# Kernel tuning notes

Measured on AMD Instinct MI355X. Metric: run time of the kernel, lower is better.

## Reference

```python
import jax, jax.numpy as jnp
import numpy as np

N, T, E, E2 = 10000, 32, 320000, 160000
D, H = 128, 128
SLOPE = 0.01  # LeakyReLU negative slope (args.relu)


def _lstm_dir(x, mask, Wih, Whh, b, reverse):
    # x: [N,T,D], mask: [N,T] int; returns final hidden [N,H] honoring per-seq lengths
    xs = jnp.swapaxes(x, 0, 1)                                 # [T,N,D]
    ms = jnp.swapaxes(mask, 0, 1)[..., None].astype(x.dtype)   # [T,N,1]
    Hh = Whh.shape[1]
    h0 = jnp.zeros((x.shape[0], Hh), x.dtype)

    def step(carry, tm):
        h, c = carry
        xt, mt = tm
        g = xt @ Wih.T + h @ Whh.T + b                         # [N,4H], torch gate order i,f,g,o
        i, f, gg, o = jnp.split(g, 4, axis=-1)
        i, f, o = jax.nn.sigmoid(i), jax.nn.sigmoid(f), jax.nn.sigmoid(o)
        c_new = f * c + i * jnp.tanh(gg)
        h_new = o * jnp.tanh(c_new)
        h = mt * h_new + (1.0 - mt) * h
        c = mt * c_new + (1.0 - mt) * c
        return (h, c), None

    (h, _), _ = jax.lax.scan(step, (h0, h0), (xs, ms), reverse=reverse)
    return h


def _sage(h, src, dst, Wself, Wneigh, b):
    # DGL SAGEConv, mean aggregator: h@W_self + mean_neigh(h)@W_neigh + b
    n = h.shape[0]
    msum = jax.ops.segment_sum(h[src], dst, num_segments=n)
    deg = jax.ops.segment_sum(jnp.ones((src.shape[0],), h.dtype), dst, num_segments=n)
    neigh = msum / jnp.maximum(deg, 1.0)[:, None]
    return h @ Wself + neigh @ Wneigh + b


def setup_inputs():
    key = jax.random.key(0)
    ks = jax.random.split(key, 40)
    f = lambda i, shape: jax.random.normal(ks[i], shape, jnp.float32) * 0.05
    return dict(
        inputs_s=jax.random.randint(ks[0], (N, T), 0, 128, jnp.int32),
        inputs_sm=jnp.ones((N, T), jnp.int32),
        inputs_c=jax.random.randint(ks[1], (N,), 0, 101, jnp.int32),
        inputs_co=jax.random.randint(ks[2], (N,), 0, 92, jnp.int32),
        inputs_sl=jax.random.randint(ks[3], (N,), 0, 6, jnp.int32),
        inputs_ip=jax.random.normal(ks[4], (N, 32), jnp.float32),
        blk_src=jax.random.randint(ks[5], (E,), 0, N, jnp.int32),
        blk_dst=jax.random.randint(ks[6], (E,), 0, N, jnp.int32),
        e_src=jax.random.randint(ks[7], (E2,), 0, N, jnp.int32),
        e_dst=jax.random.randint(ks[8], (E2,), 0, N, jnp.int32),
        emb_url=f(9, (128, D)), emb_cat=f(10, (101, D)), emb_cou=f(11, (92, D)), emb_sl_t=f(12, (6, D)),
        Wih_f=f(13, (4 * D, D)), Whh_f=f(14, (4 * D, D)), b_f=f(15, (4 * D,)),
        Wih_b=f(16, (4 * D, D)), Whh_b=f(17, (4 * D, D)), b_b=f(18, (4 * D,)),
        fc_lstm_W=f(19, (2 * D, D)), fc_lstm_b=f(20, (D,)),
        attnlin_W=f(21, (H, H)), attn_W=f(22, (H, 1)), attn_b=f(23, (1,)),
        W0_self=f(24, (4, D, H)), W0_neigh=f(25, (4, D, H)), b0=f(26, (4, H)),
        Wip_self=f(27, (32, H)), Wip_neigh=f(28, (32, H)), bip=f(29, (H,)),
        W1_self=f(30, (5, H, H)), W1_neigh=f(31, (5, H, H)), b1=f(32, (5, H)),
        fc_W=f(33, (2 * H, H)), fc_b=f(34, (H,)),
        fco_W=f(35, (H, 2)), fco_b=f(36, (2,)),
    )


def reference(inputs_s, inputs_sm, inputs_c, inputs_co, inputs_sl, inputs_ip,
              blk_src, blk_dst, e_src, e_dst,
              emb_url, emb_cat, emb_cou, emb_sl_t,
              Wih_f, Whh_f, b_f, Wih_b, Whh_b, b_b,
              fc_lstm_W, fc_lstm_b, attnlin_W, attn_W, attn_b,
              W0_self, W0_neigh, b0, Wip_self, Wip_neigh, bip,
              W1_self, W1_neigh, b1, fc_W, fc_b, fco_W, fco_b):
    lrelu = lambda x: jax.nn.leaky_relu(x, SLOPE)
    # --- URL encoder: embed -> bi-LSTM -> fc (dropout is identity in eval) ---
    xu = emb_url[inputs_s]                                      # [N,T,D]
    hf = _lstm_dir(xu, inputs_sm, Wih_f, Whh_f, b_f, False)     # fwd final hidden
    hb = _lstm_dir(xu, inputs_sm, Wih_b, Whh_b, b_b, True)      # bwd final hidden
    vec_url = lrelu(jnp.concatenate([hf, hb], 1) @ fc_lstm_W + fc_lstm_b)
    # --- six-stream (here five: no rules) SAGE stacks over shared blocks ---
    h4 = jnp.stack([vec_url, emb_cat[inputs_c], emb_cou[inputs_co], emb_sl_t[inputs_sl]])  # [4,N,D]
    sage_v = jax.vmap(_sage, in_axes=(0, None, None, 0, 0, 0))
    h4 = lrelu(sage_v(h4, blk_src, blk_dst, W0_self, W0_neigh, b0))
    hip = lrelu(_sage(inputs_ip, blk_src, blk_dst, Wip_self, Wip_neigh, bip))
    hs = jnp.concatenate([h4, hip[None]], 0)                    # [5,N,H]
    hs = lrelu(sage_v(hs, blk_src, blk_dst, W1_self, W1_neigh, b1))
    hs = jnp.transpose(hs, (1, 0, 2))                           # [N,5,H]
    # --- attention fusion across streams ---
    z = jnp.einsum('nsh,ho->nso', hs, attnlin_W)                # attn_linear(h_stack)
    a = jax.nn.softmax(jnp.einsum('nso,om->nsm', z, attn_W) + attn_b, axis=1)  # [N,5,1]
    h = jnp.sum(z * a, axis=1)                                  # [N,H]
    # --- per-edge gather-concat-MLP scoring (apply_edges) ---
    cat = jnp.concatenate([h[e_src], h[e_dst]], 1)              # [E2,2H]
    score = lrelu(cat @ fc_W + fc_b) @ fco_W + fco_b            # [E2,2]
    a_src = a[e_src][..., 0]                                    # [E2,5]
    attn_e = jnp.stack([a_src, a_src], axis=1)                  # [E2,2,5]
    return score, attn_e
```

## Files before the change

### kernel.cpp

```cpp
#include <hip/hip_runtime.h>
#include <hip/hip_bf16.h>
#include <stdint.h>

typedef unsigned short u16;
typedef unsigned int   u32;
typedef __attribute__((ext_vector_type(8))) short short8;
typedef __attribute__((ext_vector_type(4))) float f32x4;
typedef __attribute__((ext_vector_type(2))) u32   u32x2;
typedef __attribute__((ext_vector_type(4))) u32   u32x4;

#define DEV static __device__ __forceinline__

constexpr int N_  = 10000;
constexpr int T_  = 32;
constexpr int E_  = 320000;
constexpr int E2_ = 160000;

DEV u16 f2bf(float f) {
    union { float f; u32 u; } v; v.f = f;
    u32 u = v.u;
    return (u16)((u + 0x7fffu + ((u >> 16) & 1u)) >> 16);
}
DEV float bf2f(u16 h) {
    union { u32 u; float f; } v; v.u = ((u32)h) << 16; return v.f;
}
DEV float asf(u32 u) {
    union { u32 u; float f; } v; v.u = u; return v.f;
}
DEV u32 cvt_pk_bf16(float lo, float hi) {
    u32 r;
    asm("v_cvt_pk_bf16_f32 %0, %1, %2" : "=v"(r) : "v"(lo), "v"(hi));
    return r;
}
DEV float lrelu(float x) { return x > 0.f ? x : 0.01f * x; }

DEV float fexp2(float x) {
#if __has_builtin(__builtin_amdgcn_exp2f)
    return __builtin_amdgcn_exp2f(x);
#else
    return exp2f(x);
#endif
}
DEV float frcp(float x) {
#if __has_builtin(__builtin_amdgcn_rcpf)
    return __builtin_amdgcn_rcpf(x);
#else
    return 1.0f / x;
#endif
}
DEV float fsig(float x)  { return frcp(1.f + fexp2(-1.4426950408889634f * x)); }
DEV float ftanh_(float x){ return 1.f - 2.f * frcp(1.f + fexp2(2.8853900817779268f * x)); }

__global__ void k_xtab(const float* __restrict__ emb,
                       const float* __restrict__ WihF, const float* __restrict__ bF,
                       const float* __restrict__ WihB, const float* __restrict__ bB,
                       u16* __restrict__ xtab) {
    int sym = blockIdx.x, dir = blockIdx.y, o = threadIdx.x;
    const float* W = dir ? WihB : WihF;
    const float* b = dir ? bB : bF;
    __shared__ float er[128];
    if (o < 128) er[o] = emb[sym * 128 + o];
    __syncthreads();
    float s = b[o];
    const float4* Wr = (const float4*)(W + (size_t)o * 128);
    for (int k4 = 0; k4 < 32; k4++) {
        float4 wv = Wr[k4];
        s += er[4*k4]   * wv.x + er[4*k4+1] * wv.y
           + er[4*k4+2] * wv.z + er[4*k4+3] * wv.w;
    }
    xtab[((size_t)(dir * 128 + sym)) * 512 + o] = f2bf(s);
}

struct WtSeg { const float* W; u16* out; int Kd, Ks, Nw, tot; };
struct WtArgs {
    WtSeg seg[9];
    int* deg; float* bias5; const float* b0; const float* bip;
};
__global__ void k_wt_all(WtArgs a) {
    if (blockIdx.y == 9) {
        int gid = blockIdx.x * 256 + threadIdx.x;
        if (gid < N_) a.deg[gid] = 0;
        int b = gid - 10240;
        if (b >= 0 && b < 640) a.bias5[b] = (b < 512) ? a.b0[b] : a.bip[b - 512];
        return;
    }
    WtSeg sg = a.seg[blockIdx.y];
    int i = blockIdx.x * 256 + threadIdx.x;
    if (i >= sg.tot) return;
    int k = i % sg.Kd, n = (i / sg.Kd) % sg.Nw, s = i / (sg.Kd * sg.Nw);
    float v = (k < sg.Ks) ? sg.W[((size_t)s * sg.Ks + k) * sg.Nw + n] : 0.f;
    sg.out[i] = f2bf(v);
}

__global__ __launch_bounds__(512, 2) void k_lstm(
    const u16* __restrict__ xtab,
    const int* __restrict__ syms,
    const int* __restrict__ smask,
    const float* __restrict__ WhhF,
    const float* __restrict__ WhhB,
    u16* __restrict__ hcat)
{
    __shared__ u16 h_buf0[2048];
    __shared__ u16 h_buf1[2048];
    __shared__ int sym_l[512];
    __shared__ int msk_l[512];

    int tid = threadIdx.x;
    int w = tid >> 6, l = tid & 63, l15 = l & 15, lg = l >> 4;
    int dir = blockIdx.y;
    int n0 = blockIdx.x * 16;
    const float* Whh = dir ? WhhB : WhhF;

    for (int i = tid; i < 512; i += 512) {
        int seq = i >> 5, t = i & 31;
        sym_l[t * 16 + seq] = syms[(size_t)n0 * 32 + i];
        msk_l[t * 16 + seq] = smask[(size_t)n0 * 32 + i];
    }
    for (int i = tid; i < 2048; i += 512) h_buf0[i] = 0;

    short8 aw[4][4];
#pragma unroll
    for (int gg = 0; gg < 4; gg++)
#pragma unroll
    for (int kk = 0; kk < 4; kk++) {
        const float* p = Whh + (size_t)(128 * gg + 16 * w + l15) * 128 + 32 * kk + 8 * lg;
        const float4* pp = (const float4*)p;
        float4 x0 = pp[0], x1 = pp[1];
        short8 v;
        v[0] = (short)f2bf(x0.x); v[1] = (short)f2bf(x0.y);
        v[2] = (short)f2bf(x0.z); v[3] = (short)f2bf(x0.w);
        v[4] = (short)f2bf(x1.x); v[5] = (short)f2bf(x1.y);
        v[6] = (short)f2bf(x1.z); v[7] = (short)f2bf(x1.w);
        aw[gg][kk] = v;
    }

    float hreg[4] = {0, 0, 0, 0};
    float creg[4] = {0, 0, 0, 0};
    int jb = 16 * w + 4 * lg;
    int wsk = 2 * w + (lg >> 1);
    int wof = (wsk * 16 + l15) * 8 + 4 * (lg & 1);
    const u16* xbase = xtab + (size_t)dir * 128 * 512 + jb;
    __syncthreads();

    u32x2 xt[4];
    {
        int t0 = dir ? 31 : 0;
        int sym0 = sym_l[t0 * 16 + l15];
        const u16* xr = xbase + (size_t)sym0 * 512;
#pragma unroll
        for (int gg = 0; gg < 4; gg++) xt[gg] = *(const u32x2*)(xr + gg * 128);
    }

    auto step = [&](int st, const u16* rb, u16* wb, bool wr) {
        int t = dir ? (31 - st) : st;

        short8 bh[4];
#pragma unroll
        for (int kk = 0; kk < 4; kk++)
            bh[kk] = *(const short8*)&rb[((kk * 4 + lg) * 16 + l15) * 8];

        f32x4 acc[4];
#pragma unroll
        for (int gg = 0; gg < 4; gg++) {
            f32x4 a = { asf(xt[gg][0] << 16), asf(xt[gg][0] & 0xffff0000u),
                        asf(xt[gg][1] << 16), asf(xt[gg][1] & 0xffff0000u) };
#pragma unroll
            for (int kk = 0; kk < 4; kk++)
                a = __builtin_amdgcn_mfma_f32_16x16x32_bf16(aw[gg][kk], bh[kk], a, 0, 0, 0);
            acc[gg] = a;
        }

        if (wr) {
            int stn = st + 1;
            int tn = dir ? (31 - stn) : stn;
            int symn = sym_l[tn * 16 + l15];
            const u16* xr = xbase + (size_t)symn * 512;
#pragma unroll
            for (int gg = 0; gg < 4; gg++) xt[gg] = *(const u32x2*)(xr + gg * 128);
        }

        int mt_i = msk_l[t * 16 + l15];
        bool mb = mt_i != 0;
#pragma unroll
        for (int r = 0; r < 4; r++) {
            float i_ = fsig(acc[0][r]), f_ = fsig(acc[1][r]);
            float g_ = ftanh_(acc[2][r]), o_ = fsig(acc[3][r]);
            float cn = f_ * creg[r] + i_ * g_;
            float hn = o_ * ftanh_(cn);
            hreg[r] = mb ? hn : hreg[r];
            creg[r] = mb ? cn : creg[r];
        }
        if (wr) {
            u32x2 pk;
            pk[0] = cvt_pk_bf16(hreg[0], hreg[1]);
            pk[1] = cvt_pk_bf16(hreg[2], hreg[3]);
            *(u32x2*)&wb[wof] = pk;
            asm volatile("s_waitcnt lgkmcnt(0)" ::: "memory");
            __builtin_amdgcn_s_barrier();
        }
    };

    for (int st2 = 0; st2 < 15; st2++) {
        step(2 * st2,     h_buf0, h_buf1, true);
        step(2 * st2 + 1, h_buf1, h_buf0, true);
    }
    step(30, h_buf0, h_buf1, true);
    step(31, h_buf1, h_buf0, false);

    {
        u32x2 pk;
        pk[0] = cvt_pk_bf16(hreg[0], hreg[1]);
        pk[1] = cvt_pk_bf16(hreg[2], hreg[3]);
        *(u32x2*)&hcat[(size_t)(n0 + l15) * 256 + dir * 128 + jb] = pk;
    }
}

template<int ACT, int DUAL>
__global__ __launch_bounds__(256) void k_gemm(
    const u16* __restrict__ A1, int lda1, int soA1,
    const u16* __restrict__ A2, int lda2, int soA2,
    const u16* __restrict__ B1, int soB1,
    const u16* __restrict__ B2, int soB2,
    const float* __restrict__ bias, int soBias,
    u16* __restrict__ C, int ldc, int soC, int M, int K)
{
    int s = blockIdx.y;
    A1 += (size_t)s * soA1;
    if (DUAL) A2 += (size_t)s * soA2;
    B1 += (size_t)s * soB1;
    if (DUAL) B2 += (size_t)s * soB2;
    if (bias) bias += (size_t)s * soBias;
    C += (size_t)s * soC;

    int tid = threadIdx.x;
    int w = tid >> 6, l = tid & 63, l15 = l & 15, lg = l >> 4;
    int mbase = blockIdx.x * 64 + w * 16;
    int arow = mbase + l15; if (arow >= M) arow = M - 1;

    f32x4 acc[8];
#pragma unroll
    for (int nt = 0; nt < 8; nt++) {
        float bv = bias ? bias[16 * nt + l15] : 0.f;
        acc[nt] = (f32x4){bv, bv, bv, bv};
    }
    for (int k0 = 0; k0 < K; k0 += 32) {
        int k = k0 + 8 * lg;
        short8 a1 = *(const short8*)&A1[(size_t)arow * lda1 + k];
        short8 a2;
        if (DUAL) a2 = *(const short8*)&A2[(size_t)arow * lda2 + k];
#pragma unroll
        for (int nt = 0; nt < 8; nt++) {
            short8 b1 = *(const short8*)&B1[(size_t)(16 * nt + l15) * K + k];
            acc[nt] = __builtin_amdgcn_mfma_f32_16x16x32_bf16(a1, b1, acc[nt], 0, 0, 0);
            if (DUAL) {
                short8 b2 = *(const short8*)&B2[(size_t)(16 * nt + l15) * K + k];
                acc[nt] = __builtin_amdgcn_mfma_f32_16x16x32_bf16(a2, b2, acc[nt], 0, 0, 0);
            }
        }
    }
#pragma unroll
    for (int nt = 0; nt < 8; nt++)
#pragma unroll
    for (int r = 0; r < 4; r++) {
        int m = mbase + 4 * lg + r;
        if (m < M) {
            float v = acc[nt][r];
            if (ACT == 1) v = lrelu(v);
            C[(size_t)m * ldc + 16 * nt + l15] = f2bf(v);
        }
    }
}

__global__ __launch_bounds__(256) void k_fcpack(
    const u16* __restrict__ hcat, const u16* __restrict__ Bt,
    const float* __restrict__ bias, u16* __restrict__ F0,
    const int* __restrict__ ic, const int* __restrict__ ico,
    const int* __restrict__ isl, const float* __restrict__ ip,
    const float* __restrict__ ecat, const float* __restrict__ ecou,
    const float* __restrict__ esl, int M)
{
    if (blockIdx.y == 1) {
        int gid = blockIdx.x * 256 + threadIdx.x;
        const int TOT = N_ * 416;
        for (int i = gid; i < TOT; i += 40192) {
            int n = i / 416, c = i - n * 416;
            float v;
            if (c < 128)      v = ecat[(size_t)ic[n]  * 128 + c];
            else if (c < 256) v = ecou[(size_t)ico[n] * 128 + (c - 128)];
            else if (c < 384) v = esl [(size_t)isl[n] * 128 + (c - 256)];
            else              v = ip  [(size_t)n * 32 + (c - 384)];
            F0[(size_t)n * 544 + 128 + c] = f2bf(v);
        }
        return;
    }
    int tid = threadIdx.x;
    int w = tid >> 6, l = tid & 63, l15 = l & 15, lg = l >> 4;
    int mbase = blockIdx.x * 64 + w * 16;
    int arow = mbase + l15; if (arow >= M) arow = M - 1;

    f32x4 acc[8];
#pragma unroll
    for (int nt = 0; nt < 8; nt++) {
        float bv = bias[16 * nt + l15];
        acc[nt] = (f32x4){bv, bv, bv, bv};
    }
    for (int k0 = 0; k0 < 256; k0 += 32) {
        int k = k0 + 8 * lg;
        short8 a1 = *(const short8*)&hcat[(size_t)arow * 256 + k];
#pragma unroll
        for (int nt = 0; nt < 8; nt++) {
            short8 b1 = *(const short8*)&Bt[(size_t)(16 * nt + l15) * 256 + k];
            acc[nt] = __builtin_amdgcn_mfma_f32_16x16x32_bf16(a1, b1, acc[nt], 0, 0, 0);
        }
    }
#pragma unroll
    for (int nt = 0; nt < 8; nt++)
#pragma unroll
    for (int r = 0; r < 4; r++) {
        int m = mbase + 4 * lg + r;
        if (m < M)
            F0[(size_t)m * 544 + 16 * nt + l15] = f2bf(lrelu(acc[nt][r]));
    }
}

__global__ void k_hist(const int* __restrict__ dst, int E, int* __restrict__ deg) {
    int e = blockIdx.x * 256 + threadIdx.x;
    if (e < E) atomicAdd(&deg[dst[e]], 1);
}
__global__ void k_scan(const int* __restrict__ deg, int* __restrict__ rowptr,
                       int* __restrict__ cursor, int n) {
    __shared__ int part[1024];
    int tid = threadIdx.x;
    const int CH = 10;
    int base = tid * CH;
    int s = 0;
#pragma unroll
    for (int i = 0; i < CH; i++) { int idx = base + i; if (idx < n) s += deg[idx]; }
    part[tid] = s; __syncthreads();
    for (int off = 1; off < 1024; off <<= 1) {
        int v = (tid >= off) ? part[tid - off] : 0;
        __syncthreads();
        part[tid] += v;
        __syncthreads();
    }
    int run = part[tid] - s;
    for (int i = 0; i < CH; i++) {
        int idx = base + i;
        if (idx < n) { rowptr[idx] = run; cursor[idx] = run; run += deg[idx]; }
    }
    if (tid == 1023) rowptr[n] = part[1023];
}
__global__ void k_fill(const int* __restrict__ src, const int* __restrict__ dst, int E,
                       int* __restrict__ cursor, int* __restrict__ colsrc) {
    int e = blockIdx.x * 256 + threadIdx.x;
    if (e < E) {
        int pos = atomicAdd(&cursor[dst[e]], 1);
        colsrc[pos] = src[e];
    }
}

__global__ __launch_bounds__(256) void k_agg(const u16* __restrict__ F, int C,
                                             const int* __restrict__ rowptr,
                                             const int* __restrict__ colsrc,
                                             u16* __restrict__ out, int N) {
    int w = threadIdx.x >> 6, l = threadIdx.x & 63;
    int n = blockIdx.x * 4 + w;
    if (n >= N) return;
    int chunks = C >> 3;
    int c0 = l, c1 = l + 64;
    bool has1 = c1 < chunks;
    float a0[8] = {0,0,0,0,0,0,0,0}, a1[8] = {0,0,0,0,0,0,0,0};
    int beg = rowptr[n], end = rowptr[n + 1];

    auto accum = [&](u32x4 v, float* a) {
#pragma unroll
        for (int j = 0; j < 4; j++) {
            u32 u = v[j];
            a[2*j]   += asf(u << 16);
            a[2*j+1] += asf(u & 0xffff0000u);
        }
    };

    int e = beg;
    for (; e + 8 <= end; e += 8) {
        const u32x4* rp[8];
#pragma unroll
        for (int j = 0; j < 8; j++)
            rp[j] = (const u32x4*)(F + (size_t)colsrc[e + j] * C);
        u32x4 v[8];
#pragma unroll
        for (int j = 0; j < 8; j++) v[j] = rp[j][c0];
        if (has1) {
            u32x4 u[8];
#pragma unroll
            for (int j = 0; j < 8; j++) u[j] = rp[j][c1];
#pragma unroll
            for (int j = 0; j < 8; j++) accum(v[j], a0);
#pragma unroll
            for (int j = 0; j < 8; j++) accum(u[j], a1);
        } else {
#pragma unroll
            for (int j = 0; j < 8; j++) accum(v[j], a0);
        }
    }
    for (; e + 4 <= end; e += 4) {
        const u32x4* rp[4];
#pragma unroll
        for (int j = 0; j < 4; j++)
            rp[j] = (const u32x4*)(F + (size_t)colsrc[e + j] * C);
        u32x4 v[4];
#pragma unroll
        for (int j = 0; j < 4; j++) v[j] = rp[j][c0];
        if (has1) {
            u32x4 u[4];
#pragma unroll
            for (int j = 0; j < 4; j++) u[j] = rp[j][c1];
#pragma unroll
            for (int j = 0; j < 4; j++) accum(v[j], a0);
#pragma unroll
            for (int j = 0; j < 4; j++) accum(u[j], a1);
        } else {
#pragma unroll
            for (int j = 0; j < 4; j++) accum(v[j], a0);
        }
    }
    for (; e < end; e++) {
        const u32x4* rp = (const u32x4*)(F + (size_t)colsrc[e] * C);
        accum(rp[c0], a0);
        if (has1) accum(rp[c1], a1);
    }

    int dg = end - beg; if (dg < 1) dg = 1;
    float inv = 1.f / (float)dg;
    u32x4 o0;
#pragma unroll
    for (int j = 0; j < 4; j++)
        o0[j] = (u32)f2bf(a0[2*j] * inv) | ((u32)f2bf(a0[2*j+1] * inv) << 16);
    ((u32x4*)(out + (size_t)n * C))[c0] = o0;
    if (has1) {
        u32x4 o1;
#pragma unroll
        for (int j = 0; j < 4; j++)
            o1[j] = (u32)f2bf(a1[2*j] * inv) | ((u32)f2bf(a1[2*j+1] * inv) << 16);
        ((u32x4*)(out + (size_t)n * C))[c1] = o1;
    }
}

__global__ __launch_bounds__(320) void k_zattn(
    const u16* __restrict__ H1,
    const u16* __restrict__ Bt,
    const float* __restrict__ attnW,
    float* __restrict__ aOut,
    u16* __restrict__ hT)
{
    constexpr int ZP = 136;
    __shared__ u16 zl[80 * ZP];
    int tid = threadIdx.x;
    int w = tid >> 6, l = tid & 63, l15 = l & 15, lg = l >> 4;
    int rbase = blockIdx.x * 80 + w * 16;

    f32x4 acc[8];
#pragma unroll
    for (int nt = 0; nt < 8; nt++) acc[nt] = (f32x4){0.f, 0.f, 0.f, 0.f};
    for (int k0 = 0; k0 < 128; k0 += 32) {
        int k = k0 + 8 * lg;
        short8 a1 = *(const short8*)&H1[(size_t)(rbase + l15) * 128 + k];
#pragma unroll
        for (int nt = 0; nt < 8; nt++) {
            short8 b1 = *(const short8*)&Bt[(size_t)(16 * nt + l15) * 128 + k];
            acc[nt] = __builtin_amdgcn_mfma_f32_16x16x32_bf16(a1, b1, acc[nt], 0, 0, 0);
        }
    }
#pragma unroll
    for (int nt = 0; nt < 8; nt++)
#pragma unroll
    for (int r = 0; r < 4; r++)
        zl[(w * 16 + 4 * lg + r) * ZP + 16 * nt + l15] = f2bf(acc[nt][r]);
    __syncthreads();

    if (tid < 256) {
        int node = tid >> 4;
        int j = tid & 15;
        int d0 = j * 8;
        float4 wa0 = *(const float4*)(attnW + d0);
        float4 wa1 = *(const float4*)(attnW + d0 + 4);
        float z[5][8], lgt[5];
#pragma unroll
        for (int s = 0; s < 5; s++) {
            const u16* zr = &zl[(node * 5 + s) * ZP + d0];
            u32x4 v = *(const u32x4*)zr;
#pragma unroll
            for (int q = 0; q < 4; q++) {
                z[s][2*q]   = asf(v[q] << 16);
                z[s][2*q+1] = asf(v[q] & 0xffff0000u);
            }
            float p = z[s][0]*wa0.x + z[s][1]*wa0.y + z[s][2]*wa0.z + z[s][3]*wa0.w
                    + z[s][4]*wa1.x + z[s][5]*wa1.y + z[s][6]*wa1.z + z[s][7]*wa1.w;
#pragma unroll
            for (int m = 1; m < 16; m <<= 1) p += __shfl_xor(p, m, 64);
            lgt[s] = p;
        }
        float mx = lgt[0];
#pragma unroll
        for (int s = 1; s < 5; s++) mx = fmaxf(mx, lgt[s]);
        float ex[5], sum = 0.f;
#pragma unroll
        for (int s = 0; s < 5; s++) { ex[s] = __expf(lgt[s] - mx); sum += ex[s]; }
        float inv = 1.f / sum;
        float a[5];
#pragma unroll
        for (int s = 0; s < 5; s++) a[s] = ex[s] * inv;
        float h[8] = {0,0,0,0,0,0,0,0};
#pragma unroll
        for (int s = 0; s < 5; s++)
#pragma unroll
            for (int q = 0; q < 8; q++) h[q] += a[s] * z[s][q];
        int gn = blockIdx.x * 16 + node;
        u32x4 o;
#pragma unroll
        for (int q = 0; q < 4; q++) o[q] = cvt_pk_bf16(h[2*q], h[2*q+1]);
        *(u32x4*)&hT[(size_t)gn * 128 + d0] = o;
        if (j == 0) {
#pragma unroll
            for (int s = 0; s < 5; s++) aOut[(size_t)gn * 5 + s] = a[s];
        }
    }
}

__global__ __launch_bounds__(256) void k_edge(const u16* __restrict__ hT,
                                              const int* __restrict__ esrc,
                                              const int* __restrict__ edst,
                                              const u16* __restrict__ fcWt,
                                              const float* __restrict__ fcb,
                                              const float* __restrict__ fcoW,
                                              const float* __restrict__ fcob,
                                              const float* __restrict__ aA,
                                              float* __restrict__ score,
                                              float* __restrict__ attne,
                                              int E2) {
    int tid = threadIdx.x;
    int w = tid >> 6, l = tid & 63, l15 = l & 15, lg = l >> 4;
    int eb = (blockIdx.x * 4 + w) * 16;
    int arow = eb + l15; if (arow >= E2) arow = E2 - 1;
    int sn = esrc[arow], dn = edst[arow];

    f32x4 acc[8];
#pragma unroll
    for (int nt = 0; nt < 8; nt++) {
        float bv = fcb[16 * nt + l15];
        acc[nt] = (f32x4){bv, bv, bv, bv};
    }
#pragma unroll
    for (int kk = 0; kk < 8; kk++) {
        int k = 32 * kk + 8 * lg;
        const u16* ap = (k < 128) ? &hT[(size_t)sn * 128 + k]
                                  : &hT[(size_t)dn * 128 + (k - 128)];
        short8 a = *(const short8*)ap;
#pragma unroll
        for (int nt = 0; nt < 8; nt++) {
            short8 b = *(const short8*)&fcWt[(size_t)(16 * nt + l15) * 256 + k];
            acc[nt] = __builtin_amdgcn_mfma_f32_16x16x32_bf16(a, b, acc[nt], 0, 0, 0);
        }
    }
    float p0[4] = {0,0,0,0}, p1[4] = {0,0,0,0};
#pragma unroll
    for (int nt = 0; nt < 8; nt++) {
        int c = 16 * nt + l15;
        float w0 = fcoW[c * 2], w1 = fcoW[c * 2 + 1];
#pragma unroll
        for (int r = 0; r < 4; r++) {
            float hd = lrelu(acc[nt][r]);
            p0[r] += hd * w0; p1[r] += hd * w1;
        }
    }
#pragma unroll
    for (int m = 1; m < 16; m <<= 1) {
#pragma unroll
        for (int r = 0; r < 4; r++) {
            p0[r] += __shfl_xor(p0[r], m, 64);
            p1[r] += __shfl_xor(p1[r], m, 64);
        }
    }
    if (l15 == 0) {
        float b0v = fcob[0], b1v = fcob[1];
#pragma unroll
        for (int r = 0; r < 4; r++) {
            int e = eb + 4 * lg + r;
            if (e < E2) {
                score[(size_t)e * 2 + 0] = p0[r] + b0v;
                score[(size_t)e * 2 + 1] = p1[r] + b1v;
            }
        }
    }
#pragma unroll
    for (int pass = 0; pass < 3; pass++) {
        int idx = pass * 64 + l;
        if (idx < 160) {
            int e = eb + idx / 10;
            int j = idx % 10;
            int s = esrc[e];
            attne[(size_t)e * 10 + j] = aA[(size_t)s * 5 + (j >= 5 ? j - 5 : j)];
        }
    }
}

extern "C" void kernel_launch(void* const* d_in, const int* in_sizes, int n_in,
                              void* d_out, int out_size, void* d_ws, size_t ws_size,
                              hipStream_t stream) {
    const int* inp_s   = (const int*)d_in[0];
    const int* inp_sm  = (const int*)d_in[1];
    const int* inp_c   = (const int*)d_in[2];
    const int* inp_co  = (const int*)d_in[3];
    const int* inp_sl  = (const int*)d_in[4];
    const float* inp_ip = (const float*)d_in[5];
    const int* blk_src = (const int*)d_in[6];
    const int* blk_dst = (const int*)d_in[7];
    const int* e_src   = (const int*)d_in[8];
    const int* e_dst   = (const int*)d_in[9];
    const float* emb_url = (const float*)d_in[10];
    const float* emb_cat = (const float*)d_in[11];
    const float* emb_cou = (const float*)d_in[12];
    const float* emb_sl  = (const float*)d_in[13];
    const float* Wih_f = (const float*)d_in[14];
    const float* Whh_f = (const float*)d_in[15];
    const float* b_f   = (const float*)d_in[16];
    const float* Wih_b = (const float*)d_in[17];
    const float* Whh_b = (const float*)d_in[18];
    const float* b_b   = (const float*)d_in[19];
    const float* fc_lstm_W = (const float*)d_in[20];
    const float* fc_lstm_b = (const float*)d_in[21];
    const float* attnlin_W = (const float*)d_in[22];
    const float* attn_W    = (const float*)d_in[23];
    const float* W0_self  = (const float*)d_in[25];
    const float* W0_neigh = (const float*)d_in[26];
    const float* b0       = (const float*)d_in[27];
    const float* Wip_self  = (const float*)d_in[28];
    const float* Wip_neigh = (const float*)d_in[29];
    const float* bip       = (const float*)d_in[30];
    const float* W1_self  = (const float*)d_in[31];
    const float* W1_neigh = (const float*)d_in[32];
    const float* b1       = (const float*)d_in[33];
    const float* fc_W  = (const float*)d_in[34];
    const float* fc_b  = (const float*)d_in[35];
    const float* fco_W = (const float*)d_in[36];
    const float* fco_b = (const float*)d_in[37];

    char* ws = (char*)d_ws;
    size_t off = 0;
    auto alloc = [&](size_t bytes) -> char* {
        char* p = ws + off;
        off += (bytes + 255) & ~(size_t)255;
        return p;
    };
    u16* xtab      = (u16*)alloc((size_t)2 * 128 * 512 * 2);
    u16* hcat      = (u16*)alloc((size_t)N_ * 256 * 2);
    u16* wt_fclstm = (u16*)alloc((size_t)128 * 256 * 2);
    u16* wt_w05s   = (u16*)alloc((size_t)5 * 128 * 128 * 2);
    u16* wt_w05n   = (u16*)alloc((size_t)5 * 128 * 128 * 2);
    u16* wt_w1s    = (u16*)alloc((size_t)5 * 128 * 128 * 2);
    u16* wt_w1n    = (u16*)alloc((size_t)5 * 128 * 128 * 2);
    u16* wt_attn   = (u16*)alloc((size_t)128 * 128 * 2);
    u16* wt_fc     = (u16*)alloc((size_t)128 * 256 * 2);
    float* bias5   = (float*)alloc((size_t)5 * 128 * 4);
    u16* F0        = (u16*)alloc((size_t)N_ * 544 * 2);
    u16* NEI       = (u16*)alloc((size_t)N_ * 640 * 2);
    u16* F1        = (u16*)alloc((size_t)N_ * 640 * 2);
    u16* H1        = (u16*)alloc((size_t)N_ * 640 * 2);
    u16* hT        = (u16*)alloc((size_t)N_ * 128 * 2);
    float* aA      = (float*)alloc((size_t)N_ * 5 * 4);
    int* deg       = (int*)alloc((size_t)N_ * 4);
    int* rowptr    = (int*)alloc((size_t)(N_ + 1) * 4);
    int* cursor    = (int*)alloc((size_t)N_ * 4);
    int* colsrc    = (int*)alloc((size_t)E_ * 4);
    (void)ws_size; (void)in_sizes; (void)n_in; (void)out_size;

    float* out_score = (float*)d_out;
    float* out_attne = out_score + (size_t)2 * E2_;

    k_xtab<<<dim3(128, 2), dim3(512), 0, stream>>>(emb_url, Wih_f, b_f, Wih_b, b_b, xtab);
    {
        WtArgs a;
        a.seg[0] = {fc_lstm_W, wt_fclstm,            256, 256, 128, 1 * 128 * 256};
        a.seg[1] = {W0_self,   wt_w05s,              128, 128, 128, 4 * 128 * 128};
        a.seg[2] = {W0_neigh,  wt_w05n,              128, 128, 128, 4 * 128 * 128};
        a.seg[3] = {Wip_self,  wt_w05s + 4 * 16384,  128,  32, 128, 1 * 128 * 128};
        a.seg[4] = {Wip_neigh, wt_w05n + 4 * 16384,  128,  32, 128, 1 * 128 * 128};
        a.seg[5] = {W1_self,   wt_w1s,               128, 128, 128, 5 * 128 * 128};
        a.seg[6] = {W1_neigh,  wt_w1n,               128, 128, 128, 5 * 128 * 128};
        a.seg[7] = {attnlin_W, wt_attn,              128, 128, 128, 1 * 128 * 128};
        a.seg[8] = {fc_W,      wt_fc,                256, 256, 128, 1 * 128 * 256};
        a.deg = deg; a.bias5 = bias5; a.b0 = b0; a.bip = bip;
        k_wt_all<<<dim3((5 * 128 * 128 + 255) / 256, 10), dim3(256), 0, stream>>>(a);
    }

    k_hist<<<dim3((E_ + 255) / 256), dim3(256), 0, stream>>>(blk_dst, E_, deg);
    k_scan<<<dim3(1), dim3(1024), 0, stream>>>(deg, rowptr, cursor, N_);
    k_fill<<<dim3((E_ + 255) / 256), dim3(256), 0, stream>>>(blk_src, blk_dst, E_, cursor, colsrc);

    k_lstm<<<dim3(N_ / 16, 2), dim3(512), 0, stream>>>(xtab, inp_s, inp_sm, Whh_f, Whh_b, hcat);

    k_fcpack<<<dim3((N_ + 63) / 64, 2), dim3(256), 0, stream>>>(
        hcat, wt_fclstm, fc_lstm_b, F0,
        inp_c, inp_co, inp_sl, inp_ip, emb_cat, emb_cou, emb_sl, N_);

    k_agg<<<dim3(N_ / 4), dim3(256), 0, stream>>>(F0, 544, rowptr, colsrc, NEI, N_);
    k_gemm<1, 1><<<dim3((N_ + 63) / 64, 5), dim3(256), 0, stream>>>(
        F0, 544, 128, NEI, 544, 128, wt_w05s, 128 * 128, wt_w05n, 128 * 128,
        bias5, 128, F1, 640, 128, N_, 128);

    k_agg<<<dim3(N_ / 4), dim3(256), 0, stream>>>(F1, 640, rowptr, colsrc, NEI, N_);
    k_gemm<1, 1><<<dim3((N_ + 63) / 64, 5), dim3(256), 0, stream>>>(
        F1, 640, 128, NEI, 640, 128, wt_w1s, 128 * 128, wt_w1n, 128 * 128,
        b1, 128, H1, 640, 128, N_, 128);

    k_zattn<<<dim3(N_ / 16), dim3(320), 0, stream>>>(H1, wt_attn, attn_W, aA, hT);

    k_edge<<<dim3(E2_ / 64), dim3(256), 0, stream>>>(hT, e_src, e_dst, wt_fc, fc_b,
                                                     fco_W, fco_b, aA,
                                                     out_score, out_attne, E2_);
}
```

Measured before the change: 596.1 us.

## Split neighbor aggregation across four waves per node and skip LSTM masking when all-ones

k_agg now gives each node a whole 256-thread block. Its four waves stride over the edge list and their partial sums are reduced through shared memory, where before one wave handled one node. This is meant to raise memory-level parallelism for gathers over average degree 32, at the cost of a shared-memory reduction and a block barrier per node. The LSTM also checks whether the block has any zero mask entry and, if none, runs a step variant with no per-step mask load or select. That second path is general, not tied to the test inputs, because it only takes the mask-free route when every entry is nonzero.

```diff
diff --git a/kernel.cpp b/kernel.cpp
--- a/kernel.cpp
+++ b/kernel.cpp
@@ -4,6 +4,7 @@
 
 typedef unsigned short u16;
 typedef unsigned int   u32;
+typedef unsigned long long u64;
 typedef __attribute__((ext_vector_type(8))) short short8;
 typedef __attribute__((ext_vector_type(4))) float f32x4;
 typedef __attribute__((ext_vector_type(2))) u32   u32x2;
@@ -104,6 +105,7 @@
     __shared__ u16 h_buf1[2048];
     __shared__ int sym_l[512];
     __shared__ int msk_l[512];
+    __shared__ int anymask;
 
     int tid = threadIdx.x;
     int w = tid >> 6, l = tid & 63, l15 = l & 15, lg = l >> 4;
@@ -111,12 +113,17 @@
     int n0 = blockIdx.x * 16;
     const float* Whh = dir ? WhhB : WhhF;
 
+    if (tid == 0) anymask = 0;
+    int m0 = 0;
     for (int i = tid; i < 512; i += 512) {
         int seq = i >> 5, t = i & 31;
+        int mv = smask[(size_t)n0 * 32 + i];
         sym_l[t * 16 + seq] = syms[(size_t)n0 * 32 + i];
-        msk_l[t * 16 + seq] = smask[(size_t)n0 * 32 + i];
+        msk_l[t * 16 + seq] = mv;
+        m0 |= (mv == 0);
     }
     for (int i = tid; i < 2048; i += 512) h_buf0[i] = 0;
+    if (__ballot(m0) != 0ull && l == 0) anymask = 1;
 
     short8 aw[4][4];
 #pragma unroll
@@ -141,6 +148,7 @@
     int wof = (wsk * 16 + l15) * 8 + 4 * (lg & 1);
     const u16* xbase = xtab + (size_t)dir * 128 * 512 + jb;
     __syncthreads();
+    bool masked = anymask != 0;
 
     u32x2 xt[4];
     {
@@ -151,7 +159,7 @@
         for (int gg = 0; gg < 4; gg++) xt[gg] = *(const u32x2*)(xr + gg * 128);
     }
 
-    auto step = [&](int st, const u16* rb, u16* wb, bool wr) {
+    auto step = [&](int st, const u16* rb, u16* wb, bool wr, bool usemask) {
         int t = dir ? (31 - st) : st;
 
         short8 bh[4];
@@ -179,16 +187,27 @@
             for (int gg = 0; gg < 4; gg++) xt[gg] = *(const u32x2*)(xr + gg * 128);
         }
 
-        int mt_i = msk_l[t * 16 + l15];
-        bool mb = mt_i != 0;
-#pragma unroll
-        for (int r = 0; r < 4; r++) {
-            float i_ = fsig(acc[0][r]), f_ = fsig(acc[1][r]);
-            float g_ = ftanh_(acc[2][r]), o_ = fsig(acc[3][r]);
-            float cn = f_ * creg[r] + i_ * g_;
-            float hn = o_ * ftanh_(cn);
-            hreg[r] = mb ? hn : hreg[r];
-            creg[r] = mb ? cn : creg[r];
+        if (usemask) {
+            int mt_i = msk_l[t * 16 + l15];
+            bool mb = mt_i != 0;
+#pragma unroll
+            for (int r = 0; r < 4; r++) {
+                float i_ = fsig(acc[0][r]), f_ = fsig(acc[1][r]);
+                float g_ = ftanh_(acc[2][r]), o_ = fsig(acc[3][r]);
+                float cn = f_ * creg[r] + i_ * g_;
+                float hn = o_ * ftanh_(cn);
+                hreg[r] = mb ? hn : hreg[r];
+                creg[r] = mb ? cn : creg[r];
+            }
+        } else {
+#pragma unroll
+            for (int r = 0; r < 4; r++) {
+                float i_ = fsig(acc[0][r]), f_ = fsig(acc[1][r]);
+                float g_ = ftanh_(acc[2][r]), o_ = fsig(acc[3][r]);
+                float cn = f_ * creg[r] + i_ * g_;
+                hreg[r] = o_ * ftanh_(cn);
+                creg[r] = cn;
+            }
         }
         if (wr) {
             u32x2 pk;
@@ -200,12 +219,21 @@
         }
     };
 
-    for (int st2 = 0; st2 < 15; st2++) {
-        step(2 * st2,     h_buf0, h_buf1, true);
-        step(2 * st2 + 1, h_buf1, h_buf0, true);
-    }
-    step(30, h_buf0, h_buf1, true);
-    step(31, h_buf1, h_buf0, false);
+    if (masked) {
+        for (int st2 = 0; st2 < 15; st2++) {
+            step(2 * st2,     h_buf0, h_buf1, true, true);
+            step(2 * st2 + 1, h_buf1, h_buf0, true, true);
+        }
+        step(30, h_buf0, h_buf1, true, true);
+        step(31, h_buf1, h_buf0, false, true);
+    } else {
+        for (int st2 = 0; st2 < 15; st2++) {
+            step(2 * st2,     h_buf0, h_buf1, true, false);
+            step(2 * st2 + 1, h_buf1, h_buf0, true, false);
+        }
+        step(30, h_buf0, h_buf1, true, false);
+        step(31, h_buf1, h_buf0, false, false);
+    }
 
     {
         u32x2 pk;
@@ -363,9 +391,10 @@
                                              const int* __restrict__ rowptr,
                                              const int* __restrict__ colsrc,
                                              u16* __restrict__ out, int N) {
-    int w = threadIdx.x >> 6, l = threadIdx.x & 63;
-    int n = blockIdx.x * 4 + w;
-    if (n >= N) return;
+    __shared__ float red[4][640];
+    int n = blockIdx.x;
+    int tid = threadIdx.x;
+    int w = tid >> 6, l = tid & 63;
     int chunks = C >> 3;
     int c0 = l, c1 = l + 64;
     bool has1 = c1 < chunks;
@@ -381,68 +410,47 @@
         }
     };
 
-    int e = beg;
-    for (; e + 8 <= end; e += 8) {
-        const u32x4* rp[8];
-#pragma unroll
-        for (int j = 0; j < 8; j++)
-            rp[j] = (const u32x4*)(F + (size_t)colsrc[e + j] * C);
-        u32x4 v[8];
-#pragma unroll
-        for (int j = 0; j < 8; j++) v[j] = rp[j][c0];
+    int e = beg + w;
+    for (; e + 4 < end; e += 8) {
+        const u32x4* r0 = (const u32x4*)(F + (size_t)colsrc[e] * C);
+        const u32x4* r1 = (const u32x4*)(F + (size_t)colsrc[e + 4] * C);
+        u32x4 v0 = r0[c0], v1 = r1[c0];
         if (has1) {
-            u32x4 u[8];
-#pragma unroll
-            for (int j = 0; j < 8; j++) u[j] = rp[j][c1];
-#pragma unroll
-            for (int j = 0; j < 8; j++) accum(v[j], a0);
-#pragma unroll
-            for (int j = 0; j < 8; j++) accum(u[j], a1);
+            u32x4 u0 = r0[c1], u1 = r1[c1];
+            accum(v0, a0); accum(v1, a0);
+            accum(u0, a1); accum(u1, a1);
         } else {
-#pragma unroll
-            for (int j = 0; j < 8; j++) accum(v[j], a0);
-        }
-    }
-    for (; e + 4 <= end; e += 4) {
-        const u32x4* rp[4];
-#pragma unroll
-        for (int j = 0; j < 4; j++)
-            rp[j] = (const u32x4*)(F + (size_t)colsrc[e + j] * C);
-        u32x4 v[4];
-#pragma unroll
-        for (int j = 0; j < 4; j++) v[j] = rp[j][c0];
-        if (has1) {
-            u32x4 u[4];
-#pragma unroll
-            for (int j = 0; j < 4; j++) u[j] = rp[j][c1];
-#pragma unroll
-            for (int j = 0; j < 4; j++) accum(v[j], a0);
-#pragma unroll
-            for (int j = 0; j < 4; j++) accum(u[j], a1);
-        } else {
-#pragma unroll
-            for (int j = 0; j < 4; j++) accum(v[j], a0);
-        }
-    }
-    for (; e < end; e++) {
-        const u32x4* rp = (const u32x4*)(F + (size_t)colsrc[e] * C);
-        accum(rp[c0], a0);
-        if (has1) accum(rp[c1], a1);
-    }
+            accum(v0, a0); accum(v1, a0);
+        }
+    }
+    if (e < end) {
+        const u32x4* r0 = (const u32x4*)(F + (size_t)colsrc[e] * C);
+        accum(r0[c0], a0);
+        if (has1) accum(r0[c1], a1);
+    }
+
+    *(float4*)&red[w][8 * c0]     = (float4){a0[0], a0[1], a0[2], a0[3]};
+    *(float4*)&red[w][8 * c0 + 4] = (float4){a0[4], a0[5], a0[6], a0[7]};
+    if (has1) {
+        *(float4*)&red[w][8 * c1]     = (float4){a1[0], a1[1], a1[2], a1[3]};
+        *(float4*)&red[w][8 * c1 + 4] = (float4){a1[4], a1[5], a1[6], a1[7]};
+    }
+    __syncthreads();
 
     int dg = end - beg; if (dg < 1) dg = 1;
     float inv = 1.f / (float)dg;
-    u32x4 o0;
-#pragma unroll
-    for (int j = 0; j < 4; j++)
-        o0[j] = (u32)f2bf(a0[2*j] * inv) | ((u32)f2bf(a0[2*j+1] * inv) << 16);
-    ((u32x4*)(out + (size_t)n * C))[c0] = o0;
-    if (has1) {
-        u32x4 o1;
-#pragma unroll
-        for (int j = 0; j < 4; j++)
-            o1[j] = (u32)f2bf(a1[2*j] * inv) | ((u32)f2bf(a1[2*j+1] * inv) << 16);
-        ((u32x4*)(out + (size_t)n * C))[c1] = o1;
+    int hc = C >> 2;
+    if (tid < hc) {
+        float4 s0 = *(const float4*)&red[0][4 * tid];
+        float4 s1 = *(const float4*)&red[1][4 * tid];
+        float4 s2 = *(const float4*)&red[2][4 * tid];
+        float4 s3 = *(const float4*)&red[3][4 * tid];
+        float x = (s0.x + s1.x + s2.x + s3.x) * inv;
+        float y = (s0.y + s1.y + s2.y + s3.y) * inv;
+        float z = (s0.z + s1.z + s2.z + s3.z) * inv;
+        float wv = (s0.w + s1.w + s2.w + s3.w) * inv;
+        u32x2 pk; pk[0] = cvt_pk_bf16(x, y); pk[1] = cvt_pk_bf16(z, wv);
+        *(u32x2*)&out[(size_t)n * C + 4 * tid] = pk;
     }
 }
 
@@ -703,12 +711,12 @@
         hcat, wt_fclstm, fc_lstm_b, F0,
         inp_c, inp_co, inp_sl, inp_ip, emb_cat, emb_cou, emb_sl, N_);
 
-    k_agg<<<dim3(N_ / 4), dim3(256), 0, stream>>>(F0, 544, rowptr, colsrc, NEI, N_);
+    k_agg<<<dim3(N_), dim3(256), 0, stream>>>(F0, 544, rowptr, colsrc, NEI, N_);
     k_gemm<1, 1><<<dim3((N_ + 63) / 64, 5), dim3(256), 0, stream>>>(
         F0, 544, 128, NEI, 544, 128, wt_w05s, 128 * 128, wt_w05n, 128 * 128,
         bias5, 128, F1, 640, 128, N_, 128);
 
-    k_agg<<<dim3(N_ / 4), dim3(256), 0, stream>>>(F1, 640, rowptr, colsrc, NEI, N_);
+    k_agg<<<dim3(N_), dim3(256), 0, stream>>>(F1, 640, rowptr, colsrc, NEI, N_);
     k_gemm<1, 1><<<dim3((N_ + 63) / 64, 5), dim3(256), 0, stream>>>(
         F1, 640, 128, NEI, 640, 128, wt_w1s, 128 * 128, wt_w1n, 128 * 128,
         b1, 128, H1, 640, 128, N_, 128);
```

Measured after the change: 576.1 us. 3.4% less time.
